# Kernel optimization log

Hardware: AMD Instinct MI355X
Metric: run time of the kernel (lower is better)

## Reference

```python
import jax, jax.numpy as jnp
import numpy as np

NUM_NODES = 50000
NUM_HYPEREDGES = 10000
NUM_INCIDENCES = 800000
CHANNELS = 256
NEG_SLOPE = 0.01  # torch leaky_relu default negative_slope


def setup_inputs() -> dict:
    key = jax.random.key(0)
    k_n, k_e, k_emb, k_cw, k_lw, k_lb = jax.random.split(key, 6)
    node_idx = jax.random.randint(k_n, (NUM_INCIDENCES,), 0, NUM_NODES, dtype=jnp.int32)
    edge_idx = jax.random.randint(k_e, (NUM_INCIDENCES,), 0, NUM_HYPEREDGES, dtype=jnp.int32)
    edge_index = jnp.stack([node_idx, edge_idx], axis=0)  # [2, nnz] incidence list
    s = 1.0 / np.sqrt(CHANNELS).astype(np.float32)
    emb = jax.random.normal(k_emb, (NUM_NODES, CHANNELS), jnp.float32)  # Node2Vec embedding table
    conv_w = jax.random.normal(k_cw, (CHANNELS, CHANNELS), jnp.float32) * s  # HypergraphConv.lin (no bias)
    conv_b = jnp.zeros((CHANNELS,), jnp.float32)  # HypergraphConv.bias
    lin_w = jax.random.normal(k_lw, (CHANNELS, CHANNELS), jnp.float32) * s
    lin_b = jax.random.normal(k_lb, (CHANNELS,), jnp.float32) * s
    return {"emb": emb, "conv_w": conv_w, "conv_b": conv_b,
            "lin_w": lin_w, "lin_b": lin_b, "edge_index": edge_index}


def reference(emb, conv_w, conv_b, lin_w, lin_b, edge_index):
    node_idx, edge_idx = edge_index[0], edge_index[1]
    # HypergraphConv (use_attention=False): X' = D^-1 H B^-1 H^T (X W^T) + b
    x = emb @ conv_w.T  # [N, C]
    ones = jnp.ones((NUM_INCIDENCES,), x.dtype)
    D = jax.ops.segment_sum(ones, node_idx, num_segments=NUM_NODES)       # node degree
    Dinv = jnp.where(D > 0, 1.0 / D, 0.0)
    B = jax.ops.segment_sum(ones, edge_idx, num_segments=NUM_HYPEREDGES)  # hyperedge degree
    Binv = jnp.where(B > 0, 1.0 / B, 0.0)
    # node -> hyperedge aggregation
    e = jax.ops.segment_sum(x[node_idx], edge_idx, num_segments=NUM_HYPEREDGES) * Binv[:, None]  # [E, C]
    # hyperedge -> node aggregation
    n = jax.ops.segment_sum(e[edge_idx], node_idx, num_segments=NUM_NODES) * Dinv[:, None] + conv_b  # [N, C]
    y = jax.nn.leaky_relu(n, NEG_SLOPE)
    g = y.T @ y  # [C, C] Gram
    out = jax.nn.leaky_relu(g @ lin_w.T + lin_b, NEG_SLOPE)
    return out
```

## Files before the change

kernel.cpp:

```cpp
#include <hip/hip_runtime.h>

#define N_NODES 50000
#define N_EDGES 10000
#define NNZ     800000
#define C       256
#define SLOPE   0.01f
#define KTOT    50176
#define KCHUNK  512
#define NZB     98
#define MPAD    10048
#define NHALF   25000

#define NB      250
#define EB_E    40
#define EB_N    200
#define CHUNK   3125
#define CAP     6000
#define MP_E    576
#define MP_N    1408

#define EAGG_G  314
#define NAGG_G  1568

#define OFF_CC_E    0
#define OFF_CC_N    1024
#define OFF_CUR_E   2048
#define OFF_CUR_N   3072
#define ZERO_BYTES  4096
#define OFF_DEG_E0  4096
#define OFF_DEG_E1  45056
#define OFF_DEG_N   86016
#define OFF_CB_E    286720
#define OFF_CB_N    288768
#define OFF_RS_N    290816
#define OFF_RS_E    491520
#define OFF_BUF_E   532480
#define OFF_BUF_N   3732480
#define OFF_CSR_E   6932480
#define OFF_CSR_N   8820480
#define OFF_EMBH    13308672
#define OFF_YT      13308672
#define OFF_E2      44144640
#define OFF_CWH     49289216
#define OFF_PART    49420288
#define OFF_EACCP   OFF_PART

typedef __attribute__((ext_vector_type(8))) short short8;
typedef __attribute__((ext_vector_type(4))) float floatx4;

static __device__ __forceinline__ unsigned short f2bf(float f) {
    unsigned int u = __float_as_uint(f);
    u = (u + 0x7fffu + ((u >> 16) & 1u)) >> 16;
    return (unsigned short)u;
}

static __device__ __forceinline__ void acc_bf8(const uint4 d, float* a) {
    a[0] += __uint_as_float(d.x << 16);
    a[1] += __uint_as_float(d.x & 0xffff0000u);
    a[2] += __uint_as_float(d.y << 16);
    a[3] += __uint_as_float(d.y & 0xffff0000u);
    a[4] += __uint_as_float(d.z << 16);
    a[5] += __uint_as_float(d.z & 0xffff0000u);
    a[6] += __uint_as_float(d.w << 16);
    a[7] += __uint_as_float(d.w & 0xffff0000u);
}

static __device__ __forceinline__ void idx8(const uint4 pk, int* ix) {
    ix[0] = (int)(pk.x & 0xffffu); ix[1] = (int)(pk.x >> 16);
    ix[2] = (int)(pk.y & 0xffffu); ix[3] = (int)(pk.y >> 16);
    ix[4] = (int)(pk.z & 0xffffu); ix[5] = (int)(pk.z >> 16);
    ix[6] = (int)(pk.w & 0xffffu); ix[7] = (int)(pk.w >> 16);
}

static __device__ __forceinline__ unsigned bfadd2(unsigned x, unsigned y) {
    float lx = __uint_as_float(x << 16), hx = __uint_as_float(x & 0xffff0000u);
    float ly = __uint_as_float(y << 16), hy = __uint_as_float(y & 0xffff0000u);
    return (unsigned)f2bf(lx + ly) | ((unsigned)f2bf(hx + hy) << 16);
}
static __device__ __forceinline__ uint4 bfadd8(uint4 x, uint4 y) {
    x.x = bfadd2(x.x, y.x); x.y = bfadd2(x.y, y.y);
    x.z = bfadd2(x.z, y.z); x.w = bfadd2(x.w, y.w);
    return x;
}

__global__ __launch_bounds__(256) void zero_kernel(float4* __restrict__ p, int n4) {
    int i = blockIdx.x * 256 + threadIdx.x;
    if (i < n4) p[i] = make_float4(0.f, 0.f, 0.f, 0.f);
}

#define PREP_EMB_BLOCKS 6251
#define PREP_CW_BLOCKS  32
__global__ __launch_bounds__(256) void prep_kernel(const float4* __restrict__ emb4,
                                                   uint4* __restrict__ embh4,
                                                   const float4* __restrict__ cw4,
                                                   uint4* __restrict__ cwh4,
                                                   const int* __restrict__ node_idx,
                                                   const int* __restrict__ edge_idx,
                                                   int* __restrict__ cc_e,
                                                   int* __restrict__ cc_n) {
    __shared__ int he[NB], hn[NB];
    int b = blockIdx.x, tid = threadIdx.x;
    if (b < PREP_EMB_BLOCKS) {
        int i = b * 256 + tid;
        if (i >= 1600032) return;
        uint4 o = {0u, 0u, 0u, 0u};
        if (i < 1600000) {
            float4 f0 = emb4[2 * i], f1 = emb4[2 * i + 1];
            o.x = f2bf(f0.x) | ((unsigned)f2bf(f0.y) << 16);
            o.y = f2bf(f0.z) | ((unsigned)f2bf(f0.w) << 16);
            o.z = f2bf(f1.x) | ((unsigned)f2bf(f1.y) << 16);
            o.w = f2bf(f1.z) | ((unsigned)f2bf(f1.w) << 16);
        }
        int node = i >> 5, c = i & 31;
        embh4[((size_t)(c >> 3) * 50001 + node) * 8 + (c & 7)] = o;
    } else if (b < PREP_EMB_BLOCKS + PREP_CW_BLOCKS) {
        int i = (b - PREP_EMB_BLOCKS) * 256 + tid;
        float4 f0 = cw4[2 * i], f1 = cw4[2 * i + 1];
        uint4 o;
        o.x = f2bf(f0.x) | ((unsigned)f2bf(f0.y) << 16);
        o.y = f2bf(f0.z) | ((unsigned)f2bf(f0.w) << 16);
        o.z = f2bf(f1.x) | ((unsigned)f2bf(f1.y) << 16);
        o.w = f2bf(f1.z) | ((unsigned)f2bf(f1.w) << 16);
        cwh4[i] = o;
    } else {
        int base = (b - PREP_EMB_BLOCKS - PREP_CW_BLOCKS) * CHUNK;
        for (int i = tid; i < NB; i += 256) { he[i] = 0; hn[i] = 0; }
        __syncthreads();
        for (int i = tid; i < CHUNK; i += 256) {
            atomicAdd(&he[edge_idx[base + i] / EB_E], 1);
            atomicAdd(&hn[node_idx[base + i] / EB_N], 1);
        }
        __syncthreads();
        for (int k = tid; k < NB; k += 256) {
            if (he[k]) atomicAdd(&cc_e[k], he[k]);
            if (hn[k]) atomicAdd(&cc_n[k], hn[k]);
        }
    }
}

__global__ __launch_bounds__(256) void coarse_scan_kernel(const int* __restrict__ cc_e,
                                                          const int* __restrict__ cc_n,
                                                          int* __restrict__ cb_e,
                                                          int* __restrict__ cb_n) {
    __shared__ int tmp[256];
    int tid = threadIdx.x;
    int v = (tid < NB) ? cc_e[tid] : 0;
    tmp[tid] = v;
    __syncthreads();
    for (int off = 1; off < 256; off <<= 1) {
        int t = (tid >= off) ? tmp[tid - off] : 0;
        __syncthreads();
        tmp[tid] += t;
        __syncthreads();
    }
    if (tid < NB) cb_e[tid + 1] = tmp[tid];
    if (tid == 0) cb_e[0] = 0;
    __syncthreads();
    v = (tid < NB) ? cc_n[tid] : 0;
    tmp[tid] = v;
    __syncthreads();
    for (int off = 1; off < 256; off <<= 1) {
        int t = (tid >= off) ? tmp[tid - off] : 0;
        __syncthreads();
        tmp[tid] += t;
        __syncthreads();
    }
    if (tid < NB) cb_n[tid + 1] = tmp[tid];
    if (tid == 0) cb_n[0] = 0;
}

__global__ __launch_bounds__(256) void bucket_scatter_kernel(const int* __restrict__ node_idx,
                                                             const int* __restrict__ edge_idx,
                                                             const int* __restrict__ cb_e,
                                                             const int* __restrict__ cb_n,
                                                             int* __restrict__ cur_e,
                                                             int* __restrict__ cur_n,
                                                             int* __restrict__ buf_e,
                                                             int* __restrict__ buf_n) {
    __shared__ int he[NB], hn[NB], be[NB], bn[NB];
    int tid = threadIdx.x;
    int base = blockIdx.x * CHUNK;
    for (int i = tid; i < NB; i += 256) { he[i] = 0; hn[i] = 0; }
    __syncthreads();
    int pe[13], pn[13];
    #pragma unroll
    for (int k = 0; k < 13; k++) {
        int i = tid + k * 256;
        if (i < CHUNK) {
            int e = edge_idx[base + i], v = node_idx[base + i];
            int ke = e / EB_E, kn = v / EB_N;
            pe[k] = (ke << 12) | atomicAdd(&he[ke], 1);
            pn[k] = (kn << 12) | atomicAdd(&hn[kn], 1);
        }
    }
    __syncthreads();
    for (int k = tid; k < NB; k += 256) {
        int c = he[k];
        be[k] = cb_e[k] + (c ? atomicAdd(&cur_e[k], c) : 0);
        int cn = hn[k];
        bn[k] = cb_n[k] + (cn ? atomicAdd(&cur_n[k], cn) : 0);
    }
    __syncthreads();
    #pragma unroll
    for (int k = 0; k < 13; k++) {
        int i = tid + k * 256;
        if (i < CHUNK) {
            int e = edge_idx[base + i], v = node_idx[base + i];
            int ke = pe[k] >> 12, oe = pe[k] & 4095;
            buf_e[be[ke] + oe] = (v << 7) | ((e - ke * EB_E) * 2 + (v >= NHALF ? 1 : 0));
            int kn = pn[k] >> 12, on = pn[k] & 4095;
            buf_n[bn[kn] + on] = (e << 8) | (v - kn * EB_N);
        }
    }
}

__global__ __launch_bounds__(256) void bucket_sort_kernel(const int* __restrict__ buf_e,
                                                          const int* __restrict__ buf_n,
                                                          const int* __restrict__ cb_e,
                                                          const int* __restrict__ cb_n,
                                                          unsigned short* __restrict__ csr_e,
                                                          unsigned short* __restrict__ csr_n,
                                                          int* __restrict__ rs_e,
                                                          int* __restrict__ rs_n,
                                                          int* __restrict__ deg_e0,
                                                          int* __restrict__ deg_e1,
                                                          int* __restrict__ deg_n) {
    __shared__ int A[CAP];
    __shared__ int h[EB_N], bs[EB_N], cs[EB_N];
    int tid = threadIdx.x;
    bool edgeSide = blockIdx.x < NB;
    int k = edgeSide ? blockIdx.x : blockIdx.x - NB;
    int rows = edgeSide ? EB_E : EB_N;
    int bins = edgeSide ? 2 * EB_E : EB_N;
    int shift = edgeSide ? 7 : 8;
    int mask = (1 << shift) - 1;
    int mp = edgeSide ? MP_E : MP_N;
    int sent = edgeSide ? N_NODES : N_EDGES;
    const int* cb  = edgeSide ? cb_e : cb_n;
    const int* buf = edgeSide ? buf_e : buf_n;
    unsigned short* csr = edgeSide ? csr_e : csr_n;
    int* rs  = edgeSide ? rs_e : rs_n;
    int base = cb[k];
    int base_pad = (base + k * mp + 7) & ~7;
    int cnt = cb[k + 1] - base;
    for (int i = tid; i < bins; i += 256) h[i] = 0;
    __syncthreads();
    for (int i = tid; i < cnt; i += 256) {
        int it = buf[base + i];
        if (i < CAP) A[i] = it;
        atomicAdd(&h[it & mask], 1);
    }
    __syncthreads();
    if (tid == 0) {
        int s = 0;
        for (int j = 0; j < bins; j++) { bs[j] = s; s += (h[j] + 7) & ~7; }
    }
    __syncthreads();
    for (int j = tid; j < bins; j += 256) { cs[j] = h[j]; h[j] = 0; }
    __syncthreads();
    for (int j = tid; j < rows; j += 256) {
        if (edgeSide) {
            rs[k * EB_E + j] = base_pad + bs[2 * j];
            deg_e0[k * EB_E + j] = cs[2 * j];
            deg_e1[k * EB_E + j] = cs[2 * j + 1];
        } else {
            rs[k * EB_N + j] = base_pad + bs[j];
            deg_n[k * EB_N + j] = cs[j];
        }
    }
    if (k == NB - 1) {
        if (tid == 0) rs[edgeSide ? N_EDGES : N_NODES] = NNZ;
        if (edgeSide) {
            if (tid < MPAD - N_EDGES) { deg_e0[N_EDGES + tid] = 0; deg_e1[N_EDGES + tid] = 0; }
        } else {
            for (int x = tid; x < KTOT - N_NODES; x += 256) deg_n[N_NODES + x] = 0;
        }
    }
    __syncthreads();
    for (int j = tid; j < bins; j += 256) {
        int c0 = cs[j], e0 = (c0 + 7) & ~7;
        for (int x = c0; x < e0; x++) csr[base_pad + bs[j] + x] = (unsigned short)sent;
    }
    for (int i = tid; i < cnt; i += 256) {
        int it = (i < CAP) ? A[i] : buf[base + i];
        int loc = it & mask;
        int off = bs[loc] + atomicAdd(&h[loc], 1);
        csr[base_pad + off] = (unsigned short)(it >> shift);
    }
}

__global__ __launch_bounds__(256) void edge_aggregate_kernel(const uint4* __restrict__ embh4,
                                                             const unsigned short* __restrict__ csr_e,
                                                             const int* __restrict__ rs_e,
                                                             const int* __restrict__ deg_e0,
                                                             const int* __restrict__ deg_e1,
                                                             unsigned short* __restrict__ e_accp) {
    int sid = blockIdx.x & 7, g = blockIdx.x >> 3;
    int cslice = sid & 3, half = sid >> 2;
    const uint4* __restrict__ csr4 = (const uint4*)csr_e;
    int tid = threadIdx.x;
    int group = tid >> 3, l8 = tid & 7;
    const uint4* __restrict__ tbl = embh4 + (size_t)cslice * 50001 * 8 + l8;
    int e = g * 32 + group;
    int s = rs_e[min(e, N_EDGES)];
    int d0 = deg_e0[e], d1 = deg_e1[e];
    int start = half ? s + ((d0 + 7) & ~7) : s;
    int dgh = half ? d1 : d0;
    int c0 = start >> 3, nc = (dgh + 7) >> 3;
    float a[8] = {0.f, 0.f, 0.f, 0.f, 0.f, 0.f, 0.f, 0.f};
    for (int c = c0; c < c0 + nc; c++) {
        uint4 pk = csr4[c];
        int ix[8];
        idx8(pk, ix);
        #pragma unroll
        for (int j = 0; j < 8; j++) acc_bf8(tbl[(size_t)ix[j] * 8], a);
    }
    uint4 o;
    o.x = f2bf(a[0]) | ((unsigned)f2bf(a[1]) << 16);
    o.y = f2bf(a[2]) | ((unsigned)f2bf(a[3]) << 16);
    o.z = f2bf(a[4]) | ((unsigned)f2bf(a[5]) << 16);
    o.w = f2bf(a[6]) | ((unsigned)f2bf(a[7]) << 16);
    *(uint4*)(e_accp + ((size_t)half * MPAD + e) * C + cslice * 64 + l8 * 8) = o;
}

__global__ __launch_bounds__(256) void edge_gemm_mfma_kernel(const unsigned short* __restrict__ e_accp,
                                                             const unsigned short* __restrict__ cwh,
                                                             const int* __restrict__ deg_e0,
                                                             const int* __restrict__ deg_e1,
                                                             unsigned short* __restrict__ e2h) {
    __shared__ __align__(16) unsigned short As[64 * 72];
    __shared__ __align__(16) unsigned short Bs[64 * 72];
    int i0 = blockIdx.x * 64, j0 = blockIdx.y * 64;
    int tid = threadIdx.x;
    int w = tid >> 6, lane = tid & 63;
    int col = lane & 15, quad = lane >> 4;
    floatx4 acc[4] = {};
    for (int step = 0; step < 4; step++) {
        int kb = step * 64;
        __syncthreads();
        #pragma unroll
        for (int l = 0; l < 2; l++) {
            int slot = tid + l * 256;
            int row = slot >> 3, grp = slot & 7;
            uint4 d0 = *(const uint4*)(e_accp + (size_t)(i0 + row) * C + kb + grp * 8);
            uint4 d1 = *(const uint4*)(e_accp + ((size_t)MPAD + i0 + row) * C + kb + grp * 8);
            *(uint4*)(&As[row * 72 + grp * 8]) = bfadd8(d0, d1);
            uint4 db = *(const uint4*)(cwh + (size_t)(j0 + row) * C + kb + grp * 8);
            *(uint4*)(&Bs[row * 72 + grp * 8]) = db;
        }
        __syncthreads();
        #pragma unroll
        for (int sub = 0; sub < 2; sub++) {
            short8 a = *(const short8*)(&As[(w * 16 + col) * 72 + sub * 32 + quad * 8]);
            #pragma unroll
            for (int jt = 0; jt < 4; jt++) {
                short8 b = *(const short8*)(&Bs[(jt * 16 + col) * 72 + sub * 32 + quad * 8]);
                acc[jt] = __builtin_amdgcn_mfma_f32_16x16x32_bf16(a, b, acc[jt], 0, 0, 0);
            }
        }
    }
    #pragma unroll
    for (int r = 0; r < 4; r++) {
        int m = i0 + w * 16 + quad * 4 + r;
        int dg = deg_e0[m] + deg_e1[m];
        float binv = (dg > 0) ? 1.0f / (float)dg : 0.0f;
        #pragma unroll
        for (int jt = 0; jt < 4; jt++) {
            int ch = j0 + jt * 16 + col;
            e2h[(size_t)((ch >> 6) * MPAD + m) * 64 + (ch & 63)] = f2bf(acc[jt][r] * binv);
        }
    }
}

__global__ __launch_bounds__(256) void node_aggregate_t_kernel(const uint4* __restrict__ e2h4,
                                                               const unsigned short* __restrict__ csr_n,
                                                               const int* __restrict__ rs_n,
                                                               const int* __restrict__ deg_n,
                                                               const float* __restrict__ conv_b,
                                                               unsigned short* __restrict__ yT) {
    __shared__ unsigned short T[64][33];
    int sid = blockIdx.x & 3, g = blockIdx.x >> 2;
    const uint4* __restrict__ csr4 = (const uint4*)csr_n;
    int tid = threadIdx.x;
    int group = tid >> 3, l8 = tid & 7;
    const uint4* __restrict__ tbl = e2h4 + (size_t)sid * MPAD * 8 + l8;
    int n = g * 32 + group;
    int s = rs_n[min(n, N_NODES)];
    int dg = deg_n[n];
    int c0 = s >> 3, nc = (dg + 7) >> 3;
    float4 b0 = ((const float4*)conv_b)[sid * 16 + l8 * 2];
    float4 b1 = ((const float4*)conv_b)[sid * 16 + l8 * 2 + 1];
    float a[8] = {0.f, 0.f, 0.f, 0.f, 0.f, 0.f, 0.f, 0.f};
    for (int c = c0; c < c0 + nc; c++) {
        uint4 pk = csr4[c];
        int ix[8];
        idx8(pk, ix);
        #pragma unroll
        for (int j = 0; j < 8; j++) acc_bf8(tbl[(size_t)ix[j] * 8], a);
    }
    float dinv = (dg > 0) ? 1.0f / (float)dg : 0.0f;
    float bb[8] = {b0.x, b0.y, b0.z, b0.w, b1.x, b1.y, b1.z, b1.w};
    #pragma unroll
    for (int jj = 0; jj < 8; jj++) {
        float r = a[jj] * dinv + bb[jj];
        r = (r > 0.f) ? r : SLOPE * r;
        if (n >= N_NODES) r = 0.f;
        T[l8 * 8 + jj][group] = f2bf(r);
    }
    __syncthreads();
    int rr = tid >> 2, cc = tid & 3;
    uint4 o;
    o.x = T[rr][cc * 8 + 0] | ((unsigned)T[rr][cc * 8 + 1] << 16);
    o.y = T[rr][cc * 8 + 2] | ((unsigned)T[rr][cc * 8 + 3] << 16);
    o.z = T[rr][cc * 8 + 4] | ((unsigned)T[rr][cc * 8 + 5] << 16);
    o.w = T[rr][cc * 8 + 6] | ((unsigned)T[rr][cc * 8 + 7] << 16);
    *(uint4*)(yT + (size_t)(sid * 64 + rr) * KTOT + g * 32 + cc * 8) = o;
}

__global__ __launch_bounds__(256) void gram_mfma_kernel(const unsigned short* __restrict__ yT,
                                                        float* __restrict__ part) {
    static const int PI[10] = {0, 0, 0, 0, 1, 1, 1, 2, 2, 3};
    static const int PJ[10] = {0, 1, 2, 3, 1, 2, 3, 2, 3, 3};
    __shared__ __align__(16) unsigned short As[64 * 72];
    __shared__ __align__(16) unsigned short Bs[64 * 72];
    int i0 = PI[blockIdx.x] * 64, j0 = PJ[blockIdx.x] * 64;
    bool diag = (i0 == j0);
    int kb0 = blockIdx.y * KCHUNK;
    int tid = threadIdx.x;
    int w = tid >> 6, lane = tid & 63;
    int col = lane & 15, quad = lane >> 4;
    floatx4 acc[4] = {};
    for (int step = 0; step < KCHUNK / 64; step++) {
        int kb = kb0 + step * 64;
        __syncthreads();
        #pragma unroll
        for (int l = 0; l < 2; l++) {
            int slot = tid + l * 256;
            int row = slot >> 3, grp = slot & 7;
            uint4 da = *(const uint4*)(yT + (size_t)(i0 + row) * KTOT + kb + grp * 8);
            *(uint4*)(&As[row * 72 + grp * 8]) = da;
            if (!diag) {
                uint4 db = *(const uint4*)(yT + (size_t)(j0 + row) * KTOT + kb + grp * 8);
                *(uint4*)(&Bs[row * 72 + grp * 8]) = db;
            }
        }
        __syncthreads();
        const unsigned short* Bb = diag ? As : Bs;
        #pragma unroll
        for (int sub = 0; sub < 2; sub++) {
            short8 a = *(const short8*)(&As[(w * 16 + col) * 72 + sub * 32 + quad * 8]);
            #pragma unroll
            for (int jt = 0; jt < 4; jt++) {
                short8 b = *(const short8*)(&Bb[(jt * 16 + col) * 72 + sub * 32 + quad * 8]);
                acc[jt] = __builtin_amdgcn_mfma_f32_16x16x32_bf16(a, b, acc[jt], 0, 0, 0);
            }
        }
    }
    float* slab = part + ((size_t)blockIdx.y * 10 + blockIdx.x) * 4096;
    #pragma unroll
    for (int jt = 0; jt < 4; jt++)
        #pragma unroll
        for (int r = 0; r < 4; r++)
            slab[(w * 16 + quad * 4 + r) * 64 + jt * 16 + col] = acc[jt][r];
}

__global__ __launch_bounds__(256) void greduce_out_kernel(const float* __restrict__ part,
                                                          const float* __restrict__ lin_w,
                                                          const float* __restrict__ lin_b,
                                                          float* __restrict__ out) {
    __shared__ float gs[C];
    int i = blockIdx.x, j = threadIdx.x;
    int a = i >> 6, b = j >> 6;
    int lo = min(a, b), hi = max(a, b);
    int t = lo * (7 - lo) / 2 + hi;
    int li = (a <= b) ? (i & 63) : (j & 63);
    int lj = (a <= b) ? (j & 63) : (i & 63);
    const float* p = part + (size_t)t * 4096 + li * 64 + lj;
    float s = 0.f;
    for (int z = 0; z < NZB; z++) s += p[(size_t)z * 40960];
    gs[j] = s;
    __syncthreads();
    float acc = lin_b[j];
    const float* wrow = lin_w + (size_t)j * C;
    for (int k = 0; k < C; k++) acc += gs[k] * wrow[k];
    out[(size_t)i * C + j] = (acc > 0.f) ? acc : SLOPE * acc;
}

extern "C" void kernel_launch(void* const* d_in, const int* in_sizes, int n_in,
                              void* d_out, int out_size, void* d_ws, size_t ws_size,
                              hipStream_t stream) {
    const float* emb    = (const float*)d_in[0];
    const float* conv_w = (const float*)d_in[1];
    const float* conv_b = (const float*)d_in[2];
    const float* lin_w  = (const float*)d_in[3];
    const float* lin_b  = (const float*)d_in[4];
    const int*   eidx   = (const int*)d_in[5];
    const int* node_idx = eidx;
    const int* edge_idx = eidx + NNZ;

    char* ws = (char*)d_ws;
    int* cc_e  = (int*)(ws + OFF_CC_E);
    int* cc_n  = (int*)(ws + OFF_CC_N);
    int* cur_e = (int*)(ws + OFF_CUR_E);
    int* cur_n = (int*)(ws + OFF_CUR_N);
    int* deg_e0 = (int*)(ws + OFF_DEG_E0);
    int* deg_e1 = (int*)(ws + OFF_DEG_E1);
    int* deg_n = (int*)(ws + OFF_DEG_N);
    int* cb_e  = (int*)(ws + OFF_CB_E);
    int* cb_n  = (int*)(ws + OFF_CB_N);
    int* rs_n  = (int*)(ws + OFF_RS_N);
    int* rs_e  = (int*)(ws + OFF_RS_E);
    int* buf_e = (int*)(ws + OFF_BUF_E);
    int* buf_n = (int*)(ws + OFF_BUF_N);
    unsigned short* csr_e = (unsigned short*)(ws + OFF_CSR_E);
    unsigned short* csr_n = (unsigned short*)(ws + OFF_CSR_N);
    uint4* embh4 = (uint4*)(ws + OFF_EMBH);
    unsigned short* e_accp = (unsigned short*)(ws + OFF_EACCP);
    unsigned short* e2h = (unsigned short*)(ws + OFF_E2);
    unsigned short* cwh = (unsigned short*)(ws + OFF_CWH);
    unsigned short* yT  = (unsigned short*)(ws + OFF_YT);
    float* part = (float*)(ws + OFF_PART);
    float* out = (float*)d_out;

    zero_kernel<<<1, 256, 0, stream>>>((float4*)ws, ZERO_BYTES / 16);

    prep_kernel<<<PREP_EMB_BLOCKS + PREP_CW_BLOCKS + 256, 256, 0, stream>>>(
        (const float4*)emb, embh4, (const float4*)conv_w, (uint4*)cwh,
        node_idx, edge_idx, cc_e, cc_n);

    coarse_scan_kernel<<<1, 256, 0, stream>>>(cc_e, cc_n, cb_e, cb_n);

    bucket_scatter_kernel<<<256, 256, 0, stream>>>(node_idx, edge_idx, cb_e, cb_n,
                                                   cur_e, cur_n, buf_e, buf_n);

    bucket_sort_kernel<<<2 * NB, 256, 0, stream>>>(buf_e, buf_n, cb_e, cb_n,
                                                   csr_e, csr_n, rs_e, rs_n,
                                                   deg_e0, deg_e1, deg_n);

    edge_aggregate_kernel<<<8 * EAGG_G, 256, 0, stream>>>(embh4, csr_e, rs_e,
                                                          deg_e0, deg_e1, e_accp);

    edge_gemm_mfma_kernel<<<dim3(MPAD / 64, C / 64), 256, 0, stream>>>(e_accp, cwh,
                                                                       deg_e0, deg_e1, e2h);

    node_aggregate_t_kernel<<<4 * NAGG_G, 256, 0, stream>>>((const uint4*)e2h, csr_n, rs_n,
                                                            deg_n, conv_b, yT);

    gram_mfma_kernel<<<dim3(10, NZB), 256, 0, stream>>>(yT, part);

    greduce_out_kernel<<<C, 256, 0, stream>>>(part, lin_w, lin_b, out);
}
```

Before: 258.7 us.

## Fold coarse scan into consumers, stage CSR in LDS, halve gram K-splits

Removes the single-block coarse_scan launch by recomputing the bucket prefix sums redundantly inside bucket_scatter and bucket_sort, and replaces the zero kernel with hipMemsetAsync. This cuts launch count and serialization gaps. bucket_sort now builds each bucket's padded CSR segment in shared memory and writes it out with 16-byte stores instead of scattered 2-byte global writes, falling back to the old path when the segment is too large. The gram kernel's K chunk is doubled, which halves the number of partial tiles the final reduce must sum but gives fewer blocks.

```diff
diff --git a/kernel.cpp b/kernel.cpp
--- a/kernel.cpp
+++ b/kernel.cpp
@@ -6,8 +6,8 @@
 #define C       256
 #define SLOPE   0.01f
 #define KTOT    50176
-#define KCHUNK  512
-#define NZB     98
+#define KCHUNK2 1024
+#define NZB2    49
 #define MPAD    10048
 #define NHALF   25000
 
@@ -16,6 +16,7 @@
 #define EB_N    200
 #define CHUNK   3125
 #define CAP     6000
+#define OCAP    5376
 #define MP_E    576
 #define MP_N    1408
 
@@ -30,8 +31,6 @@
 #define OFF_DEG_E0  4096
 #define OFF_DEG_E1  45056
 #define OFF_DEG_N   86016
-#define OFF_CB_E    286720
-#define OFF_CB_N    288768
 #define OFF_RS_N    290816
 #define OFF_RS_E    491520
 #define OFF_BUF_E   532480
@@ -81,11 +80,6 @@
     x.x = bfadd2(x.x, y.x); x.y = bfadd2(x.y, y.y);
     x.z = bfadd2(x.z, y.z); x.w = bfadd2(x.w, y.w);
     return x;
-}
-
-__global__ __launch_bounds__(256) void zero_kernel(float4* __restrict__ p, int n4) {
-    int i = blockIdx.x * 256 + threadIdx.x;
-    if (i < n4) p[i] = make_float4(0.f, 0.f, 0.f, 0.f);
 }
 
 #define PREP_EMB_BLOCKS 6251
@@ -138,48 +132,39 @@
     }
 }
 
-__global__ __launch_bounds__(256) void coarse_scan_kernel(const int* __restrict__ cc_e,
-                                                          const int* __restrict__ cc_n,
-                                                          int* __restrict__ cb_e,
-                                                          int* __restrict__ cb_n) {
-    __shared__ int tmp[256];
-    int tid = threadIdx.x;
-    int v = (tid < NB) ? cc_e[tid] : 0;
-    tmp[tid] = v;
-    __syncthreads();
-    for (int off = 1; off < 256; off <<= 1) {
-        int t = (tid >= off) ? tmp[tid - off] : 0;
-        __syncthreads();
-        tmp[tid] += t;
-        __syncthreads();
-    }
-    if (tid < NB) cb_e[tid + 1] = tmp[tid];
-    if (tid == 0) cb_e[0] = 0;
-    __syncthreads();
-    v = (tid < NB) ? cc_n[tid] : 0;
-    tmp[tid] = v;
-    __syncthreads();
-    for (int off = 1; off < 256; off <<= 1) {
-        int t = (tid >= off) ? tmp[tid - off] : 0;
-        __syncthreads();
-        tmp[tid] += t;
-        __syncthreads();
-    }
-    if (tid < NB) cb_n[tid + 1] = tmp[tid];
-    if (tid == 0) cb_n[0] = 0;
-}
-
 __global__ __launch_bounds__(256) void bucket_scatter_kernel(const int* __restrict__ node_idx,
                                                              const int* __restrict__ edge_idx,
-                                                             const int* __restrict__ cb_e,
-                                                             const int* __restrict__ cb_n,
+                                                             const int* __restrict__ cc_e,
+                                                             const int* __restrict__ cc_n,
                                                              int* __restrict__ cur_e,
                                                              int* __restrict__ cur_n,
                                                              int* __restrict__ buf_e,
                                                              int* __restrict__ buf_n) {
     __shared__ int he[NB], hn[NB], be[NB], bn[NB];
+    __shared__ int cbl_e[NB], cbl_n[NB], tmp[256];
     int tid = threadIdx.x;
     int base = blockIdx.x * CHUNK;
+    int v = (tid < NB) ? cc_e[tid] : 0;
+    tmp[tid] = v;
+    __syncthreads();
+    for (int off = 1; off < 256; off <<= 1) {
+        int t = (tid >= off) ? tmp[tid - off] : 0;
+        __syncthreads();
+        tmp[tid] += t;
+        __syncthreads();
+    }
+    if (tid < NB) cbl_e[tid] = tmp[tid] - v;
+    __syncthreads();
+    v = (tid < NB) ? cc_n[tid] : 0;
+    tmp[tid] = v;
+    __syncthreads();
+    for (int off = 1; off < 256; off <<= 1) {
+        int t = (tid >= off) ? tmp[tid - off] : 0;
+        __syncthreads();
+        tmp[tid] += t;
+        __syncthreads();
+    }
+    if (tid < NB) cbl_n[tid] = tmp[tid] - v;
     for (int i = tid; i < NB; i += 256) { he[i] = 0; hn[i] = 0; }
     __syncthreads();
     int pe[13], pn[13];
@@ -187,8 +172,8 @@
     for (int k = 0; k < 13; k++) {
         int i = tid + k * 256;
         if (i < CHUNK) {
-            int e = edge_idx[base + i], v = node_idx[base + i];
-            int ke = e / EB_E, kn = v / EB_N;
+            int e = edge_idx[base + i], v2 = node_idx[base + i];
+            int ke = e / EB_E, kn = v2 / EB_N;
             pe[k] = (ke << 12) | atomicAdd(&he[ke], 1);
             pn[k] = (kn << 12) | atomicAdd(&hn[kn], 1);
         }
@@ -196,28 +181,28 @@
     __syncthreads();
     for (int k = tid; k < NB; k += 256) {
         int c = he[k];
-        be[k] = cb_e[k] + (c ? atomicAdd(&cur_e[k], c) : 0);
+        be[k] = cbl_e[k] + (c ? atomicAdd(&cur_e[k], c) : 0);
         int cn = hn[k];
-        bn[k] = cb_n[k] + (cn ? atomicAdd(&cur_n[k], cn) : 0);
+        bn[k] = cbl_n[k] + (cn ? atomicAdd(&cur_n[k], cn) : 0);
     }
     __syncthreads();
     #pragma unroll
     for (int k = 0; k < 13; k++) {
         int i = tid + k * 256;
         if (i < CHUNK) {
-            int e = edge_idx[base + i], v = node_idx[base + i];
+            int e = edge_idx[base + i], v2 = node_idx[base + i];
             int ke = pe[k] >> 12, oe = pe[k] & 4095;
-            buf_e[be[ke] + oe] = (v << 7) | ((e - ke * EB_E) * 2 + (v >= NHALF ? 1 : 0));
+            buf_e[be[ke] + oe] = (v2 << 7) | ((e - ke * EB_E) * 2 + (v2 >= NHALF ? 1 : 0));
             int kn = pn[k] >> 12, on = pn[k] & 4095;
-            buf_n[bn[kn] + on] = (e << 8) | (v - kn * EB_N);
+            buf_n[bn[kn] + on] = (e << 8) | (v2 - kn * EB_N);
         }
     }
 }
 
 __global__ __launch_bounds__(256) void bucket_sort_kernel(const int* __restrict__ buf_e,
                                                           const int* __restrict__ buf_n,
-                                                          const int* __restrict__ cb_e,
-                                                          const int* __restrict__ cb_n,
+                                                          const int* __restrict__ cc_e,
+                                                          const int* __restrict__ cc_n,
                                                           unsigned short* __restrict__ csr_e,
                                                           unsigned short* __restrict__ csr_n,
                                                           int* __restrict__ rs_e,
@@ -226,7 +211,9 @@
                                                           int* __restrict__ deg_e1,
                                                           int* __restrict__ deg_n) {
     __shared__ int A[CAP];
+    __shared__ unsigned short O[OCAP];
     __shared__ int h[EB_N], bs[EB_N], cs[EB_N];
+    __shared__ int tmp[256];
     int tid = threadIdx.x;
     bool edgeSide = blockIdx.x < NB;
     int k = edgeSide ? blockIdx.x : blockIdx.x - NB;
@@ -236,13 +223,25 @@
     int mask = (1 << shift) - 1;
     int mp = edgeSide ? MP_E : MP_N;
     int sent = edgeSide ? N_NODES : N_EDGES;
-    const int* cb  = edgeSide ? cb_e : cb_n;
+    const int* cc  = edgeSide ? cc_e : cc_n;
     const int* buf = edgeSide ? buf_e : buf_n;
     unsigned short* csr = edgeSide ? csr_e : csr_n;
     int* rs  = edgeSide ? rs_e : rs_n;
-    int base = cb[k];
+    int vv = (tid < NB) ? cc[tid] : 0;
+    tmp[tid] = vv;
+    __syncthreads();
+    for (int off = 1; off < 256; off <<= 1) {
+        int t = (tid >= off) ? tmp[tid - off] : 0;
+        __syncthreads();
+        tmp[tid] += t;
+        __syncthreads();
+    }
+    __shared__ int baseSh;
+    if (tid == k) baseSh = tmp[k] - vv;
+    __syncthreads();
+    int base = baseSh;
     int base_pad = (base + k * mp + 7) & ~7;
-    int cnt = cb[k + 1] - base;
+    int cnt = cc[k];
     for (int i = tid; i < bins; i += 256) h[i] = 0;
     __syncthreads();
     for (int i = tid; i < cnt; i += 256) {
@@ -277,15 +276,31 @@
         }
     }
     __syncthreads();
-    for (int j = tid; j < bins; j += 256) {
-        int c0 = cs[j], e0 = (c0 + 7) & ~7;
-        for (int x = c0; x < e0; x++) csr[base_pad + bs[j] + x] = (unsigned short)sent;
-    }
-    for (int i = tid; i < cnt; i += 256) {
-        int it = (i < CAP) ? A[i] : buf[base + i];
-        int loc = it & mask;
-        int off = bs[loc] + atomicAdd(&h[loc], 1);
-        csr[base_pad + off] = (unsigned short)(it >> shift);
+    int psz = bs[bins - 1] + ((cs[bins - 1] + 7) & ~7);
+    if (psz <= OCAP) {
+        for (int s = tid; s < psz; s += 256) O[s] = (unsigned short)sent;
+        __syncthreads();
+        for (int i = tid; i < cnt; i += 256) {
+            int it = (i < CAP) ? A[i] : buf[base + i];
+            int loc = it & mask;
+            int off = bs[loc] + atomicAdd(&h[loc], 1);
+            O[off] = (unsigned short)(it >> shift);
+        }
+        __syncthreads();
+        uint4* dst = (uint4*)(csr + base_pad);
+        const uint4* src = (const uint4*)O;
+        for (int s = tid; s * 8 < psz; s += 256) dst[s] = src[s];
+    } else {
+        for (int j = tid; j < bins; j += 256) {
+            int c0 = cs[j], e0 = (c0 + 7) & ~7;
+            for (int x = c0; x < e0; x++) csr[base_pad + bs[j] + x] = (unsigned short)sent;
+        }
+        for (int i = tid; i < cnt; i += 256) {
+            int it = (i < CAP) ? A[i] : buf[base + i];
+            int loc = it & mask;
+            int off = bs[loc] + atomicAdd(&h[loc], 1);
+            csr[base_pad + off] = (unsigned short)(it >> shift);
+        }
     }
 }
 
@@ -425,12 +440,12 @@
     __shared__ __align__(16) unsigned short Bs[64 * 72];
     int i0 = PI[blockIdx.x] * 64, j0 = PJ[blockIdx.x] * 64;
     bool diag = (i0 == j0);
-    int kb0 = blockIdx.y * KCHUNK;
+    int kb0 = blockIdx.y * KCHUNK2;
     int tid = threadIdx.x;
     int w = tid >> 6, lane = tid & 63;
     int col = lane & 15, quad = lane >> 4;
     floatx4 acc[4] = {};
-    for (int step = 0; step < KCHUNK / 64; step++) {
+    for (int step = 0; step < KCHUNK2 / 64; step++) {
         int kb = kb0 + step * 64;
         __syncthreads();
         #pragma unroll
@@ -477,7 +492,7 @@
     int lj = (a <= b) ? (j & 63) : (i & 63);
     const float* p = part + (size_t)t * 4096 + li * 64 + lj;
     float s = 0.f;
-    for (int z = 0; z < NZB; z++) s += p[(size_t)z * 40960];
+    for (int z = 0; z < NZB2; z++) s += p[(size_t)z * 40960];
     gs[j] = s;
     __syncthreads();
     float acc = lin_b[j];
@@ -506,8 +521,6 @@
     int* deg_e0 = (int*)(ws + OFF_DEG_E0);
     int* deg_e1 = (int*)(ws + OFF_DEG_E1);
     int* deg_n = (int*)(ws + OFF_DEG_N);
-    int* cb_e  = (int*)(ws + OFF_CB_E);
-    int* cb_n  = (int*)(ws + OFF_CB_N);
     int* rs_n  = (int*)(ws + OFF_RS_N);
     int* rs_e  = (int*)(ws + OFF_RS_E);
     int* buf_e = (int*)(ws + OFF_BUF_E);
@@ -522,18 +535,16 @@
     float* part = (float*)(ws + OFF_PART);
     float* out = (float*)d_out;
 
-    zero_kernel<<<1, 256, 0, stream>>>((float4*)ws, ZERO_BYTES / 16);
+    hipMemsetAsync(ws, 0, ZERO_BYTES, stream);
 
     prep_kernel<<<PREP_EMB_BLOCKS + PREP_CW_BLOCKS + 256, 256, 0, stream>>>(
         (const float4*)emb, embh4, (const float4*)conv_w, (uint4*)cwh,
         node_idx, edge_idx, cc_e, cc_n);
 
-    coarse_scan_kernel<<<1, 256, 0, stream>>>(cc_e, cc_n, cb_e, cb_n);
-
-    bucket_scatter_kernel<<<256, 256, 0, stream>>>(node_idx, edge_idx, cb_e, cb_n,
+    bucket_scatter_kernel<<<256, 256, 0, stream>>>(node_idx, edge_idx, cc_e, cc_n,
                                                    cur_e, cur_n, buf_e, buf_n);
 
-    bucket_sort_kernel<<<2 * NB, 256, 0, stream>>>(buf_e, buf_n, cb_e, cb_n,
+    bucket_sort_kernel<<<2 * NB, 256, 0, stream>>>(buf_e, buf_n, cc_e, cc_n,
                                                    csr_e, csr_n, rs_e, rs_n,
                                                    deg_e0, deg_e1, deg_n);
 
@@ -546,7 +557,7 @@
     node_aggregate_t_kernel<<<4 * NAGG_G, 256, 0, stream>>>((const uint4*)e2h, csr_n, rs_n,
                                                             deg_n, conv_b, yT);
 
-    gram_mfma_kernel<<<dim3(10, NZB), 256, 0, stream>>>(yT, part);
+    gram_mfma_kernel<<<dim3(10, NZB2), 256, 0, stream>>>(yT, part);
 
     greduce_out_kernel<<<C, 256, 0, stream>>>(part, lin_w, lin_b, out);
 }
```

After: 249.7 us. 3.5% less time.
